# Kernel optimization log

Hardware: AMD Instinct MI355X
Metric: run time of the kernel (lower is better)

Reference implementation:

```python
import math
import jax, jax.numpy as jnp
import numpy as np

B, N, D = 32, 1025, 768
H, d = 12, 64
R = 1
S, td = 32, 2
ts = td * td          # 4
T = (N - R) // ts     # 256
U = 1
K = R + T * U         # 257
CPB_H = 32


def _cpb_buffers():
    # query positions: R registers (dummy, masked) + SxS patch grid
    qy = np.concatenate([np.zeros(R), np.repeat(np.arange(S), S)]).astype(np.float32)
    qx = np.concatenate([np.zeros(R), np.tile(np.arange(S), S)]).astype(np.float32)
    qm = np.concatenate([np.zeros(R), np.ones(S * S)]).astype(np.float32)
    # context positions: R registers (dummy) + tile centers on (S//td)x(S//td) grid
    g = S // td
    cy = np.repeat(np.arange(g), g) * td + (td - 1) / 2.0
    cx = np.tile(np.arange(g), g) * td + (td - 1) / 2.0
    ky = np.concatenate([np.zeros(R), cy]).astype(np.float32)
    kx = np.concatenate([np.zeros(R), cx]).astype(np.float32)
    km = np.concatenate([np.zeros(R), np.ones(g * g)]).astype(np.float32)
    dy = qy[:, None] - ky[None, :]
    dx = qx[:, None] - kx[None, :]
    phi = lambda t: np.sign(t) * np.log1p(np.abs(t))
    feats = np.stack([phi(dy), phi(dx)], axis=-1)  # [N, K, 2]
    mask = qm[:, None] * km[None, :]               # [N, K]
    return jnp.asarray(feats), jnp.asarray(mask)


def setup_inputs() -> dict:
    key = jax.random.key(0)
    ks = jax.random.split(key, 10)
    s = 0.02
    feats, mask = _cpb_buffers()
    return {
        "x": jax.random.normal(ks[0], (B, N, D), jnp.float32),
        "W_logit": jax.random.normal(ks[1], (U, D), jnp.float32) * s,
        "Wq": jax.random.normal(ks[2], (D, D), jnp.float32) * s,
        "Wkv": jax.random.normal(ks[3], (2 * D, D), jnp.float32) * s,
        "Wo": jax.random.normal(ks[4], (D, D), jnp.float32) * s,
        "bo": jnp.zeros((D,), jnp.float32),
        "cpb_w1": jax.random.normal(ks[5], (CPB_H, 2), jnp.float32) * 0.5,
        "cpb_b1": jax.random.normal(ks[6], (CPB_H,), jnp.float32) * 0.1,
        "cpb_w2": jax.random.normal(ks[7], (H, CPB_H), jnp.float32) * 0.1,
        "cpb_b2": jnp.zeros((H,), jnp.float32),
        "feats": feats,
        "mask": mask,
    }


def reference(x, W_logit, Wq, Wkv, Wo, bo, cpb_w1, cpb_b1, cpb_w2, cpb_b2, feats, mask):
    Bx = x.shape[0]
    # --- tiled local pooling to build compressed context ---
    patch = x[:, R:, :].reshape(Bx, S // td, td, S // td, td, D)
    tiled = patch.transpose(0, 1, 3, 2, 4, 5).reshape(Bx, T, ts, D)  # [B,T,ts,D]
    scores = jnp.einsum('btsd,ud->btsu', tiled, W_logit)             # [B,T,ts,U]
    w = jax.nn.softmax(scores.astype(jnp.float32).transpose(0, 1, 3, 2), axis=-1).astype(x.dtype)
    ctx_learn = jnp.einsum('btus,btsd->btud', w, tiled).reshape(Bx, T * U, D)
    ctx = jnp.concatenate([x[:, :R, :], ctx_learn], axis=1)          # [B,K,D]
    # --- q / kv projections ---
    q = (x @ Wq.T).reshape(Bx, N, H, d).transpose(0, 2, 1, 3)        # [B,H,N,d]
    kv = (ctx @ Wkv.T).reshape(Bx, K, 2, H, d).transpose(2, 0, 3, 1, 4)
    k, v = kv[0], kv[1]                                              # [B,H,K,d]
    # --- CPB relative position bias ---
    h = jax.nn.gelu(feats @ cpb_w1.T + cpb_b1, approximate=False)    # [N,K,32]
    bias = (h @ cpb_w2.T + cpb_b2).transpose(2, 0, 1) * mask         # [H,N,K]
    # --- SDPA with additive bias ---
    scale = 1.0 / math.sqrt(d)
    logits = jnp.einsum('bhnd,bhkd->bhnk', q, k) * scale + bias
    attn = jax.nn.softmax(logits, axis=-1)
    o = jnp.einsum('bhnk,bhkd->bhnd', attn, v).transpose(0, 2, 1, 3).reshape(Bx, N, D)
    return o @ Wo.T + bo
```

## Files before the change

### kernel.cpp

```cpp
#include <hip/hip_runtime.h>
#include <math.h>

#define BB 32
#define NN 1025
#define DDIM 768
#define HH 12
#define DHD 64
#define KC 257
#define CPBH 32

#define BT_K 320
#define BT_N 1088
#define SCALE_LOG2E 0.18033688011112042f

typedef unsigned int u32;
typedef unsigned short u16;
typedef unsigned char u8;
typedef __attribute__((ext_vector_type(8))) short s8v;
typedef __attribute__((ext_vector_type(4))) float f4v;

__device__ __forceinline__ u16 f2bf(float f) {
  union { float f; u32 u; } v; v.f = f;
  return (u16)((v.u + 0x7fffu + ((v.u >> 16) & 1u)) >> 16);
}
__device__ __forceinline__ float bf2f(u16 h) {
  union { u32 u; float f; } v; v.u = ((u32)h) << 16;
  return v.f;
}
__device__ __forceinline__ void gload16(const u16* g, u16* l) {
  __builtin_amdgcn_global_load_lds((const __attribute__((address_space(1))) void*)g,
                                   (__attribute__((address_space(3))) void*)l, 16, 0, 0);
}

__global__ __launch_bounds__(256) void cast_bf16_kernel(const float* __restrict__ s,
                                                        u16* __restrict__ d, int n8) {
  const int i = blockIdx.x * 256 + threadIdx.x;
  if (i >= n8) return;
  const float4 f0 = ((const float4*)s)[2 * i];
  const float4 f1 = ((const float4*)s)[2 * i + 1];
  s8v o;
  o[0] = (short)f2bf(f0.x); o[1] = (short)f2bf(f0.y);
  o[2] = (short)f2bf(f0.z); o[3] = (short)f2bf(f0.w);
  o[4] = (short)f2bf(f1.x); o[5] = (short)f2bf(f1.y);
  o[6] = (short)f2bf(f1.z); o[7] = (short)f2bf(f1.w);
  *(s8v*)&d[8 * (size_t)i] = o;
}

__global__ __launch_bounds__(256) void split_bf16_kernel(const float* __restrict__ s,
                                                         u16* __restrict__ dh,
                                                         u16* __restrict__ dl, int n8) {
  const int i = blockIdx.x * 256 + threadIdx.x;
  if (i >= n8) return;
  s8v oh, ol;
#pragma unroll
  for (int j = 0; j < 8; j++) {
    const float f = s[8 * (size_t)i + j];
    const u16 hb = f2bf(f);
    oh[j] = (short)hb;
    ol[j] = (short)f2bf(f - bf2f(hb));
  }
  *(s8v*)&dh[8 * (size_t)i] = oh;
  *(s8v*)&dl[8 * (size_t)i] = ol;
}

__global__ __launch_bounds__(64) void pool_ctx_kernel(const float* __restrict__ x,
                                                      const float* __restrict__ wlog,
                                                      u16* __restrict__ ctx) {
  const int bid = blockIdx.x;
  const int b = bid / KC;
  const int kk = bid % KC;
  const int lane = threadIdx.x;
  const float* xb = x + (size_t)b * NN * DDIM;
  u16* cout = ctx + ((size_t)b * KC + kk) * DDIM;
  if (kk == 0) {
    for (int c = lane; c < DDIM; c += 64) cout[c] = f2bf(xb[c]);
    return;
  }
  const int t = kk - 1;
  const int gy = t >> 4, gx = t & 15;
  const int r0 = 1 + gy * 64 + gx * 2;
  const float* xr0 = xb + (size_t)r0 * DDIM;
  float s0 = 0.f, s1 = 0.f, s2 = 0.f, s3 = 0.f;
  for (int c = lane; c < DDIM; c += 64) {
    const float w = wlog[c];
    s0 = fmaf(xr0[c], w, s0);
    s1 = fmaf(xr0[c + DDIM], w, s1);
    s2 = fmaf(xr0[c + 32 * DDIM], w, s2);
    s3 = fmaf(xr0[c + 33 * DDIM], w, s3);
  }
#pragma unroll
  for (int off = 32; off; off >>= 1) {
    s0 += __shfl_xor(s0, off);
    s1 += __shfl_xor(s1, off);
    s2 += __shfl_xor(s2, off);
    s3 += __shfl_xor(s3, off);
  }
  const float m = fmaxf(fmaxf(s0, s1), fmaxf(s2, s3));
  float e0 = expf(s0 - m), e1 = expf(s1 - m), e2 = expf(s2 - m), e3 = expf(s3 - m);
  const float inv = 1.0f / (e0 + e1 + e2 + e3);
  e0 *= inv; e1 *= inv; e2 *= inv; e3 *= inv;
  for (int c = lane; c < DDIM; c += 64) {
    cout[c] = f2bf(e0 * xr0[c] + e1 * xr0[c + DDIM] + e2 * xr0[c + 32 * DDIM] +
                   e3 * xr0[c + 33 * DDIM]);
  }
}

__global__ __launch_bounds__(256) void cpb_biasT_kernel(const float* __restrict__ feats,
                                                        const float* __restrict__ mask,
                                                        const float* __restrict__ w1,
                                                        const float* __restrict__ b1,
                                                        const float* __restrict__ w2,
                                                        const float* __restrict__ b2,
                                                        float* __restrict__ biasT) {
  const int idx = blockIdx.x * 256 + threadIdx.x;
  if (idx >= BT_K * BT_N) return;
  const int k = idx / BT_N;
  const int n = idx - k * BT_N;
  const bool valid = (k < KC) && (n < NN);
  float out[HH];
  if (valid) {
    const float2 f = *(const float2*)&feats[2 * ((size_t)n * KC + k)];
    const float mk = mask[(size_t)n * KC + k] * 1.4426950408889634f;
    float hb[CPBH];
#pragma unroll
    for (int j = 0; j < CPBH; j++) {
      const float tv = fmaf(w1[2 * j], f.x, fmaf(w1[2 * j + 1], f.y, b1[j]));
      hb[j] = 0.5f * tv * (1.0f + erff(tv * 0.70710678118654752f));
    }
#pragma unroll
    for (int h = 0; h < HH; h++) {
      float acc = b2[h];
#pragma unroll
      for (int j = 0; j < CPBH; j++) acc = fmaf(hb[j], w2[h * CPBH + j], acc);
      out[h] = acc * mk;
    }
  } else {
#pragma unroll
    for (int h = 0; h < HH; h++) out[h] = -1.0e30f;
  }
#pragma unroll
  for (int h = 0; h < HH; h++) biasT[(size_t)h * BT_K * BT_N + idx] = out[h];
}

template <int SPLIT, int WRITE_BF16, int ADD_BIAS>
__global__ __launch_bounds__(256) void gemm_mfma(const u16* __restrict__ Ah,
                                                 const u16* __restrict__ Al,
                                                 const u16* __restrict__ Bh,
                                                 const u16* __restrict__ Bl,
                                                 const float* __restrict__ bias,
                                                 float* __restrict__ Cf,
                                                 u16* __restrict__ Cb, int M, int Nout,
                                                 int nNB) {
  constexpr int BN = SPLIT ? 64 : 128;
  constexpr int NTI = SPLIT ? 2 : 4;
  __shared__ u16 AhL[128 * 32];
  __shared__ u16 BhL[BN * 32];
  __shared__ u16 AlL[SPLIT ? 128 * 32 : 8];
  __shared__ u16 BlL[SPLIT ? BN * 32 : 8];
  const int tid = threadIdx.x;
  const int w = tid >> 6, l = tid & 63;
  const int lane16 = l & 15, quad = l >> 4;
  const int nwg = (int)gridDim.x;
  const int q8 = nwg >> 3, r8 = nwg & 7;
  const int xcd = (int)blockIdx.x & 7, idx8 = (int)blockIdx.x >> 3;
  const int orig = (xcd < r8 ? xcd * (q8 + 1) : r8 * (q8 + 1) + (xcd - r8) * q8) + idx8;
  const int mb = orig / nNB;
  const int nb = orig - mb * nNB;
  const int m0 = mb * 128, n0 = nb * BN;
  const int sr = l >> 2, sc = (l & 3) * 8;
  const int ar0 = min(m0 + w * 32 + sr, M - 1);
  const int ar1 = min(m0 + w * 32 + 16 + sr, M - 1);
  const u16* ap0 = Ah + (size_t)ar0 * DDIM + sc;
  const u16* ap1 = Ah + (size_t)ar1 * DDIM + sc;
  const u16* alp0 = nullptr; const u16* alp1 = nullptr;
  const u16* bp0 = nullptr; const u16* bp1 = nullptr; const u16* blp0 = nullptr;
  if constexpr (SPLIT) {
    alp0 = Al + (size_t)ar0 * DDIM + sc;
    alp1 = Al + (size_t)ar1 * DDIM + sc;
    bp0 = Bh + (size_t)(n0 + w * 16 + sr) * DDIM + sc;
    blp0 = Bl + (size_t)(n0 + w * 16 + sr) * DDIM + sc;
  } else {
    bp0 = Bh + (size_t)(n0 + w * 32 + sr) * DDIM + sc;
    bp1 = Bh + (size_t)(n0 + w * 32 + 16 + sr) * DDIM + sc;
  }
  f4v acc[4][NTI];
#pragma unroll
  for (int mt = 0; mt < 4; mt++)
#pragma unroll
    for (int nt = 0; nt < NTI; nt++) acc[mt][nt] = (f4v){0.f, 0.f, 0.f, 0.f};
  const int mh = (w & 1) * 64;
  const int nh = (w >> 1) * (SPLIT ? 32 : 64);

  for (int k0 = 0; k0 < DDIM; k0 += 32) {
    __syncthreads();
    gload16(ap0 + k0, &AhL[(w * 32) * 32]);
    gload16(ap1 + k0, &AhL[(w * 32 + 16) * 32]);
    if constexpr (SPLIT) {
      gload16(alp0 + k0, &AlL[(w * 32) * 32]);
      gload16(alp1 + k0, &AlL[(w * 32 + 16) * 32]);
      gload16(bp0 + k0, &BhL[(w * 16) * 32]);
      gload16(blp0 + k0, &BlL[(w * 16) * 32]);
    } else {
      gload16(bp0 + k0, &BhL[(w * 32) * 32]);
      gload16(bp1 + k0, &BhL[(w * 32 + 16) * 32]);
    }
    __syncthreads();
    s8v af[4], afl[4];
#pragma unroll
    for (int mt = 0; mt < 4; mt++) {
      af[mt] = *(const s8v*)&AhL[(mh + mt * 16 + lane16) * 32 + quad * 8];
      if constexpr (SPLIT)
        afl[mt] = *(const s8v*)&AlL[(mh + mt * 16 + lane16) * 32 + quad * 8];
    }
#pragma unroll
    for (int nt = 0; nt < NTI; nt++) {
      const s8v bfh = *(const s8v*)&BhL[(nh + nt * 16 + lane16) * 32 + quad * 8];
      s8v bfl;
      if constexpr (SPLIT)
        bfl = *(const s8v*)&BlL[(nh + nt * 16 + lane16) * 32 + quad * 8];
#pragma unroll
      for (int mt = 0; mt < 4; mt++) {
        acc[mt][nt] = __builtin_amdgcn_mfma_f32_16x16x32_bf16(af[mt], bfh, acc[mt][nt], 0, 0, 0);
        if constexpr (SPLIT) {
          acc[mt][nt] = __builtin_amdgcn_mfma_f32_16x16x32_bf16(afl[mt], bfh, acc[mt][nt], 0, 0, 0);
          acc[mt][nt] = __builtin_amdgcn_mfma_f32_16x16x32_bf16(af[mt], bfl, acc[mt][nt], 0, 0, 0);
        }
      }
    }
  }
#pragma unroll
  for (int mt = 0; mt < 4; mt++)
#pragma unroll
    for (int nt = 0; nt < NTI; nt++)
#pragma unroll
      for (int r = 0; r < 4; r++) {
        const int row = m0 + mh + mt * 16 + quad * 4 + r;
        if (row < M) {
          const int col = n0 + nh + nt * 16 + lane16;
          float v = acc[mt][nt][r];
          if (ADD_BIAS) v += bias[col];
          if (WRITE_BF16) Cb[(size_t)row * Nout + col] = f2bf(v);
          else Cf[(size_t)row * Nout + col] = v;
        }
      }
}

__global__ __launch_bounds__(256) void transpose_v_kernel(const u16* __restrict__ kvb,
                                                          u16* __restrict__ vt) {
  const int bh = blockIdx.x;
  const int b = bh / HH, h = bh % HH;
  const int tid = threadIdx.x;
  const int kk = tid >> 3;
  const int c0 = (tid & 7) * 8;
  u16* dbase = vt + (((size_t)b * HH + h) * 64 + c0) * BT_K;
#pragma unroll
  for (int ch = 0; ch < 10; ch++) {
    const int k = ch * 32 + kk;
    s8v v = {0, 0, 0, 0, 0, 0, 0, 0};
    if (k < KC)
      v = *(const s8v*)(kvb + ((size_t)b * KC + k) * (2 * DDIM) + DDIM + h * DHD + c0);
#pragma unroll
    for (int j = 0; j < 8; j++) dbase[(size_t)j * BT_K + k] = (u16)v[j];
  }
}

#define PLS 72

__global__ __launch_bounds__(256, 4) void attn_mfma(const u16* qb,
                                                    const u16* __restrict__ kvb,
                                                    const u16* __restrict__ vt,
                                                    const float* __restrict__ biasT,
                                                    u16* oh, u16* __restrict__ ol) {
  __shared__ u16 KV[2][64 * 64];
  __shared__ u16 PL[4][16 * PLS];
  const int tid = threadIdx.x;
  const int w = tid >> 6, l = tid & 63;
  const int lane16 = l & 15, quad = l >> 4;
  const int r7 = lane16 & 7;
  const int nwg = (int)gridDim.x;
  const int q8 = nwg >> 3, r8 = nwg & 7;
  const int xcd = (int)blockIdx.x & 7, idx8 = (int)blockIdx.x >> 3;
  const int orig = (xcd < r8 ? xcd * (q8 + 1) : r8 * (q8 + 1) + (xcd - r8) * q8) + idx8;
  const int nb = orig % 17;
  const int hb = orig / 17;
  const int b = hb % BB, h = hb / BB;
  const int n_base = nb * 64 + w * 16;

  const u16* kvb_bh = kvb + (size_t)b * KC * (2 * DDIM) + h * DHD;
  const u16* vt_bh = vt + (((size_t)b * HH + h) * 64) * BT_K;

  const int srow = l >> 3;
  const int scol = ((l & 7) ^ srow) * 8;
  const int rbase = w * 16;

#pragma unroll
  for (int j = 0; j < 2; j++) {
    const int krow = min(rbase + j * 8 + srow, KC - 1);
    gload16(kvb_bh + (size_t)krow * (2 * DDIM) + scol, &KV[0][(rbase + j * 8) * 64]);
  }

  const int qrow = min(n_base + lane16, NN - 1);
  const u16* qp = qb + ((size_t)b * NN + qrow) * DDIM + h * DHD + quad * 8;
  const s8v qf0 = *(const s8v*)qp;
  const s8v qf1 = *(const s8v*)(qp + 32);

  __syncthreads();

  f4v S[17];
  const float* bT = biasT + (size_t)h * BT_K * BT_N + (size_t)(n_base + quad * 4);
  float mx[4] = {-3.0e38f, -3.0e38f, -3.0e38f, -3.0e38f};
#pragma unroll
  for (int ch = 0; ch < 5; ch++) {
    if (ch < 4) {
#pragma unroll
      for (int j = 0; j < 2; j++) {
        const int krow = min((ch + 1) * 64 + rbase + j * 8 + srow, KC - 1);
        gload16(kvb_bh + (size_t)krow * (2 * DDIM) + scol,
                &KV[(ch + 1) & 1][(rbase + j * 8) * 64]);
      }
    }
    const u16* KL = KV[ch & 1];
#pragma unroll
    for (int tt = 0; tt < 4; tt++) {
      const int t = ch * 4 + tt;
      if (t < 17) {
        const int row = tt * 16 + lane16;
        const s8v kf0 = *(const s8v*)&KL[row * 64 + ((quad ^ r7) * 8)];
        const s8v kf1 = *(const s8v*)&KL[row * 64 + (((quad + 4) ^ r7) * 8)];
        f4v z = {0.f, 0.f, 0.f, 0.f};
        z = __builtin_amdgcn_mfma_f32_16x16x32_bf16(qf0, kf0, z, 0, 0, 0);
        z = __builtin_amdgcn_mfma_f32_16x16x32_bf16(qf1, kf1, z, 0, 0, 0);
        const float4 bv = *(const float4*)&bT[(size_t)(t * 16 + lane16) * BT_N];
        S[t][0] = fmaf(z[0], SCALE_LOG2E, bv.x);
        S[t][1] = fmaf(z[1], SCALE_LOG2E, bv.y);
        S[t][2] = fmaf(z[2], SCALE_LOG2E, bv.z);
        S[t][3] = fmaf(z[3], SCALE_LOG2E, bv.w);
#pragma unroll
        for (int r = 0; r < 4; r++) mx[r] = fmaxf(mx[r], S[t][r]);
      }
    }
    __syncthreads();
  }

#pragma unroll
  for (int j = 0; j < 2; j++) {
    const int c = rbase + j * 8 + srow;
    gload16(vt_bh + (size_t)c * BT_K + scol, &KV[0][(rbase + j * 8) * 64]);
  }

#pragma unroll
  for (int r = 0; r < 4; r++) {
    mx[r] = fmaxf(mx[r], __shfl_xor(mx[r], 1));
    mx[r] = fmaxf(mx[r], __shfl_xor(mx[r], 2));
    mx[r] = fmaxf(mx[r], __shfl_xor(mx[r], 4));
    mx[r] = fmaxf(mx[r], __shfl_xor(mx[r], 8));
  }
  float sm[4] = {0.f, 0.f, 0.f, 0.f};
#pragma unroll
  for (int t = 0; t < 17; t++)
#pragma unroll
    for (int r = 0; r < 4; r++) {
      const float p = exp2f(S[t][r] - mx[r]);
      S[t][r] = p;
      sm[r] += p;
    }
#pragma unroll
  for (int r = 0; r < 4; r++) {
    sm[r] += __shfl_xor(sm[r], 1);
    sm[r] += __shfl_xor(sm[r], 2);
    sm[r] += __shfl_xor(sm[r], 4);
    sm[r] += __shfl_xor(sm[r], 8);
    sm[r] = 1.0f / sm[r];
  }

  f4v O[4];
#pragma unroll
  for (int nt = 0; nt < 4; nt++) O[nt] = (f4v){0.f, 0.f, 0.f, 0.f};

  __syncthreads();

  u16* PLw = PL[w];
#pragma unroll
  for (int ch = 0; ch < 5; ch++) {
    if (ch < 4) {
#pragma unroll
      for (int j = 0; j < 2; j++) {
        const int c = rbase + j * 8 + srow;
        gload16(vt_bh + (size_t)c * BT_K + (ch + 1) * 64 + scol,
                &KV[(ch + 1) & 1][(rbase + j * 8) * 64]);
      }
    }
#pragma unroll
    for (int tt = 0; tt < 4; tt++) {
      const int t = ch * 4 + tt;
#pragma unroll
      for (int r = 0; r < 4; r++) {
        float pv = 0.f;
        if (t < 17) pv = S[t][r];
        PLw[(quad * 4 + r) * PLS + tt * 16 + lane16] = f2bf(pv);
      }
    }
    const u16* VL = KV[ch & 1];
#pragma unroll
    for (int ks = 0; ks < 2; ks++) {
      const s8v a = *(const s8v*)&PLw[lane16 * PLS + ks * 32 + quad * 8];
#pragma unroll
      for (int nt = 0; nt < 4; nt++) {
        const s8v bfr =
            *(const s8v*)&VL[(nt * 16 + lane16) * 64 + (((ks * 4 + quad) ^ r7) * 8)];
        O[nt] = __builtin_amdgcn_mfma_f32_16x16x32_bf16(a, bfr, O[nt], 0, 0, 0);
      }
    }
    __syncthreads();
  }

#pragma unroll
  for (int nt = 0; nt < 4; nt++)
#pragma unroll
    for (int r = 0; r < 4; r++) {
      const int n = n_base + quad * 4 + r;
      if (n < NN) {
        const size_t idx = ((size_t)b * NN + n) * DDIM + h * DHD + nt * 16 + lane16;
        const float v = O[nt][r] * sm[r];
        const u16 hb2 = f2bf(v);
        oh[idx] = hb2;
        ol[idx] = f2bf(v - bf2f(hb2));
      }
    }
}

extern "C" void kernel_launch(void* const* d_in, const int* in_sizes, int n_in,
                              void* d_out, int out_size, void* d_ws, size_t ws_size,
                              hipStream_t stream) {
  (void)in_sizes; (void)n_in; (void)out_size; (void)ws_size;
  const float* x    = (const float*)d_in[0];
  const float* wlog = (const float*)d_in[1];
  const float* Wq   = (const float*)d_in[2];
  const float* Wkv  = (const float*)d_in[3];
  const float* Wo   = (const float*)d_in[4];
  const float* bo   = (const float*)d_in[5];
  const float* w1   = (const float*)d_in[6];
  const float* b1   = (const float*)d_in[7];
  const float* w2   = (const float*)d_in[8];
  const float* b2   = (const float*)d_in[9];
  const float* feats = (const float*)d_in[10];
  const float* mask  = (const float*)d_in[11];
  float* out = (float*)d_out;

  u8* p = (u8*)d_ws;
  u16* xb    = (u16*)(p + 0);
  u16* ctxb  = (u16*)(p + 50380800);
  u16* Wqb   = (u16*)(p + 63012864);
  u16* Wkvb  = (u16*)(p + 64192512);
  u16* Woh   = (u16*)(p + 66551808);
  u16* Wol   = (u16*)(p + 67731456);
  u16* qb    = (u16*)(p + 68911104);
  u16* kvb   = (u16*)(p + 119291904);
  u16* vt    = (u16*)(p + 144556032);
  float* biasT = (float*)(p + 160284672);

  const int nx8 = (BB * NN * DDIM) / 8;
  cast_bf16_kernel<<<dim3((nx8 + 255) / 256), dim3(256), 0, stream>>>(x, xb, nx8);
  cast_bf16_kernel<<<dim3(288), dim3(256), 0, stream>>>(Wq, Wqb, (DDIM * DDIM) / 8);
  cast_bf16_kernel<<<dim3(576), dim3(256), 0, stream>>>(Wkv, Wkvb, (2 * DDIM * DDIM) / 8);
  split_bf16_kernel<<<dim3(288), dim3(256), 0, stream>>>(Wo, Woh, Wol, (DDIM * DDIM) / 8);
  pool_ctx_kernel<<<dim3(BB * KC), dim3(64), 0, stream>>>(x, wlog, ctxb);
  cpb_biasT_kernel<<<dim3((BT_K * BT_N) / 256), dim3(256), 0, stream>>>(
      feats, mask, w1, b1, w2, b2, biasT);
  gemm_mfma<0, 1, 0><<<dim3(257 * 6), dim3(256), 0, stream>>>(
      xb, nullptr, Wqb, nullptr, nullptr, nullptr, qb, BB * NN, DDIM, 6);
  gemm_mfma<0, 1, 0><<<dim3(65 * 12), dim3(256), 0, stream>>>(
      ctxb, nullptr, Wkvb, nullptr, nullptr, nullptr, kvb, BB * KC, 2 * DDIM, 12);
  transpose_v_kernel<<<dim3(BB * HH), dim3(256), 0, stream>>>(kvb, vt);
  attn_mfma<<<dim3(17 * HH * BB), dim3(256), 0, stream>>>(qb, kvb, vt, biasT, qb, xb);
  gemm_mfma<1, 0, 1><<<dim3(257 * 12), dim3(256), 0, stream>>>(
      qb, xb, Woh, Wol, bo, out, nullptr, BB * NN, DDIM, 12);
}
```

Before: 638.4 us.

## Double-buffer GEMM LDS tiles and vectorize the pooled-context kernel

The MFMA GEMM now uses two LDS buffers per operand, issuing the global-to-LDS loads for the next K slice before computing the current one. This replaces the two barriers per iteration with one and is meant to hide load latency behind the MFMAs, at the cost of twice the shared memory, which can lower occupancy. Separately, the pooling kernel packs four context rows into a 256-thread block and uses float4 loads and ushort4 stores to cut launch granularity and memory instruction count.

```diff
diff --git a/kernel.cpp b/kernel.cpp
--- a/kernel.cpp
+++ b/kernel.cpp
@@ -63,17 +63,23 @@
   *(s8v*)&dl[8 * (size_t)i] = ol;
 }
 
-__global__ __launch_bounds__(64) void pool_ctx_kernel(const float* __restrict__ x,
-                                                      const float* __restrict__ wlog,
-                                                      u16* __restrict__ ctx) {
+__global__ __launch_bounds__(256) void pool_ctx_kernel(const float* __restrict__ x,
+                                                       const float* __restrict__ wlog,
+                                                       u16* __restrict__ ctx) {
+  const int w = threadIdx.x >> 6, lane = threadIdx.x & 63;
   const int bid = blockIdx.x;
-  const int b = bid / KC;
-  const int kk = bid % KC;
-  const int lane = threadIdx.x;
+  const int b = bid / 65;
+  const int kk = (bid % 65) * 4 + w;
+  if (kk >= KC) return;
   const float* xb = x + (size_t)b * NN * DDIM;
   u16* cout = ctx + ((size_t)b * KC + kk) * DDIM;
   if (kk == 0) {
-    for (int c = lane; c < DDIM; c += 64) cout[c] = f2bf(xb[c]);
+#pragma unroll
+    for (int u = lane; u < 192; u += 64) {
+      const float4 f = ((const float4*)xb)[u];
+      ushort4 o = {f2bf(f.x), f2bf(f.y), f2bf(f.z), f2bf(f.w)};
+      *(ushort4*)&cout[u * 4] = o;
+    }
     return;
   }
   const int t = kk - 1;
@@ -81,12 +87,17 @@
   const int r0 = 1 + gy * 64 + gx * 2;
   const float* xr0 = xb + (size_t)r0 * DDIM;
   float s0 = 0.f, s1 = 0.f, s2 = 0.f, s3 = 0.f;
-  for (int c = lane; c < DDIM; c += 64) {
-    const float w = wlog[c];
-    s0 = fmaf(xr0[c], w, s0);
-    s1 = fmaf(xr0[c + DDIM], w, s1);
-    s2 = fmaf(xr0[c + 32 * DDIM], w, s2);
-    s3 = fmaf(xr0[c + 33 * DDIM], w, s3);
+#pragma unroll
+  for (int u = lane; u < 192; u += 64) {
+    const float4 a = ((const float4*)xr0)[u];
+    const float4 bq = ((const float4*)(xr0 + DDIM))[u];
+    const float4 c = ((const float4*)(xr0 + 32 * DDIM))[u];
+    const float4 d = ((const float4*)(xr0 + 33 * DDIM))[u];
+    const float4 wv = ((const float4*)wlog)[u];
+    s0 = fmaf(a.x, wv.x, fmaf(a.y, wv.y, fmaf(a.z, wv.z, fmaf(a.w, wv.w, s0))));
+    s1 = fmaf(bq.x, wv.x, fmaf(bq.y, wv.y, fmaf(bq.z, wv.z, fmaf(bq.w, wv.w, s1))));
+    s2 = fmaf(c.x, wv.x, fmaf(c.y, wv.y, fmaf(c.z, wv.z, fmaf(c.w, wv.w, s2))));
+    s3 = fmaf(d.x, wv.x, fmaf(d.y, wv.y, fmaf(d.z, wv.z, fmaf(d.w, wv.w, s3))));
   }
 #pragma unroll
   for (int off = 32; off; off >>= 1) {
@@ -99,9 +110,18 @@
   float e0 = expf(s0 - m), e1 = expf(s1 - m), e2 = expf(s2 - m), e3 = expf(s3 - m);
   const float inv = 1.0f / (e0 + e1 + e2 + e3);
   e0 *= inv; e1 *= inv; e2 *= inv; e3 *= inv;
-  for (int c = lane; c < DDIM; c += 64) {
-    cout[c] = f2bf(e0 * xr0[c] + e1 * xr0[c + DDIM] + e2 * xr0[c + 32 * DDIM] +
-                   e3 * xr0[c + 33 * DDIM]);
+#pragma unroll
+  for (int u = lane; u < 192; u += 64) {
+    const float4 a = ((const float4*)xr0)[u];
+    const float4 bq = ((const float4*)(xr0 + DDIM))[u];
+    const float4 c = ((const float4*)(xr0 + 32 * DDIM))[u];
+    const float4 d = ((const float4*)(xr0 + 33 * DDIM))[u];
+    ushort4 o;
+    o.x = f2bf(e0 * a.x + e1 * bq.x + e2 * c.x + e3 * d.x);
+    o.y = f2bf(e0 * a.y + e1 * bq.y + e2 * c.y + e3 * d.y);
+    o.z = f2bf(e0 * a.z + e1 * bq.z + e2 * c.z + e3 * d.z);
+    o.w = f2bf(e0 * a.w + e1 * bq.w + e2 * c.w + e3 * d.w);
+    *(ushort4*)&cout[u * 4] = o;
   }
 }
 
@@ -153,10 +173,10 @@
                                                  int nNB) {
   constexpr int BN = SPLIT ? 64 : 128;
   constexpr int NTI = SPLIT ? 2 : 4;
-  __shared__ u16 AhL[128 * 32];
-  __shared__ u16 BhL[BN * 32];
-  __shared__ u16 AlL[SPLIT ? 128 * 32 : 8];
-  __shared__ u16 BlL[SPLIT ? BN * 32 : 8];
+  __shared__ u16 AhL[2][128 * 32];
+  __shared__ u16 BhL[2][BN * 32];
+  __shared__ u16 AlL[2][SPLIT ? 128 * 32 : 8];
+  __shared__ u16 BlL[2][SPLIT ? BN * 32 : 8];
   const int tid = threadIdx.x;
   const int w = tid >> 6, l = tid & 63;
   const int lane16 = l & 15, quad = l >> 4;
@@ -191,33 +211,49 @@
   const int mh = (w & 1) * 64;
   const int nh = (w >> 1) * (SPLIT ? 32 : 64);
 
+  gload16(ap0, &AhL[0][(w * 32) * 32]);
+  gload16(ap1, &AhL[0][(w * 32 + 16) * 32]);
+  if constexpr (SPLIT) {
+    gload16(alp0, &AlL[0][(w * 32) * 32]);
+    gload16(alp1, &AlL[0][(w * 32 + 16) * 32]);
+    gload16(bp0, &BhL[0][(w * 16) * 32]);
+    gload16(blp0, &BlL[0][(w * 16) * 32]);
+  } else {
+    gload16(bp0, &BhL[0][(w * 32) * 32]);
+    gload16(bp1, &BhL[0][(w * 32 + 16) * 32]);
+  }
+  __syncthreads();
+
+  int cur = 0;
   for (int k0 = 0; k0 < DDIM; k0 += 32) {
-    __syncthreads();
-    gload16(ap0 + k0, &AhL[(w * 32) * 32]);
-    gload16(ap1 + k0, &AhL[(w * 32 + 16) * 32]);
-    if constexpr (SPLIT) {
-      gload16(alp0 + k0, &AlL[(w * 32) * 32]);
-      gload16(alp1 + k0, &AlL[(w * 32 + 16) * 32]);
-      gload16(bp0 + k0, &BhL[(w * 16) * 32]);
-      gload16(blp0 + k0, &BlL[(w * 16) * 32]);
-    } else {
-      gload16(bp0 + k0, &BhL[(w * 32) * 32]);
-      gload16(bp1 + k0, &BhL[(w * 32 + 16) * 32]);
-    }
-    __syncthreads();
+    const int kn = k0 + 32;
+    if (kn < DDIM) {
+      const int nx = cur ^ 1;
+      gload16(ap0 + kn, &AhL[nx][(w * 32) * 32]);
+      gload16(ap1 + kn, &AhL[nx][(w * 32 + 16) * 32]);
+      if constexpr (SPLIT) {
+        gload16(alp0 + kn, &AlL[nx][(w * 32) * 32]);
+        gload16(alp1 + kn, &AlL[nx][(w * 32 + 16) * 32]);
+        gload16(bp0 + kn, &BhL[nx][(w * 16) * 32]);
+        gload16(blp0 + kn, &BlL[nx][(w * 16) * 32]);
+      } else {
+        gload16(bp0 + kn, &BhL[nx][(w * 32) * 32]);
+        gload16(bp1 + kn, &BhL[nx][(w * 32 + 16) * 32]);
+      }
+    }
     s8v af[4], afl[4];
 #pragma unroll
     for (int mt = 0; mt < 4; mt++) {
-      af[mt] = *(const s8v*)&AhL[(mh + mt * 16 + lane16) * 32 + quad * 8];
+      af[mt] = *(const s8v*)&AhL[cur][(mh + mt * 16 + lane16) * 32 + quad * 8];
       if constexpr (SPLIT)
-        afl[mt] = *(const s8v*)&AlL[(mh + mt * 16 + lane16) * 32 + quad * 8];
+        afl[mt] = *(const s8v*)&AlL[cur][(mh + mt * 16 + lane16) * 32 + quad * 8];
     }
 #pragma unroll
     for (int nt = 0; nt < NTI; nt++) {
-      const s8v bfh = *(const s8v*)&BhL[(nh + nt * 16 + lane16) * 32 + quad * 8];
+      const s8v bfh = *(const s8v*)&BhL[cur][(nh + nt * 16 + lane16) * 32 + quad * 8];
       s8v bfl;
       if constexpr (SPLIT)
-        bfl = *(const s8v*)&BlL[(nh + nt * 16 + lane16) * 32 + quad * 8];
+        bfl = *(const s8v*)&BlL[cur][(nh + nt * 16 + lane16) * 32 + quad * 8];
 #pragma unroll
       for (int mt = 0; mt < 4; mt++) {
         acc[mt][nt] = __builtin_amdgcn_mfma_f32_16x16x32_bf16(af[mt], bfh, acc[mt][nt], 0, 0, 0);
@@ -227,6 +263,8 @@
         }
       }
     }
+    __syncthreads();
+    cur ^= 1;
   }
 #pragma unroll
   for (int mt = 0; mt < 4; mt++)
@@ -464,7 +502,7 @@
   cast_bf16_kernel<<<dim3(288), dim3(256), 0, stream>>>(Wq, Wqb, (DDIM * DDIM) / 8);
   cast_bf16_kernel<<<dim3(576), dim3(256), 0, stream>>>(Wkv, Wkvb, (2 * DDIM * DDIM) / 8);
   split_bf16_kernel<<<dim3(288), dim3(256), 0, stream>>>(Wo, Woh, Wol, (DDIM * DDIM) / 8);
-  pool_ctx_kernel<<<dim3(BB * KC), dim3(64), 0, stream>>>(x, wlog, ctxb);
+  pool_ctx_kernel<<<dim3(BB * 65), dim3(256), 0, stream>>>(x, wlog, ctxb);
   cpb_biasT_kernel<<<dim3((BT_K * BT_N) / 256), dim3(256), 0, stream>>>(
       feats, mask, w1, b1, w2, b2, biasT);
   gemm_mfma<0, 1, 0><<<dim3(257 * 6), dim3(256), 0, stream>>>(
```

Measured after the change: 619.4 us. 1.03x faster.
